# Kernel optimization log

Measured on AMD Instinct MI355X. Metric: run time of the kernel, lower is better.

The kernel has to match this reference:

```python
import jax, jax.numpy as jnp
import numpy as np

B, S = 4, 2048
N_EMBED = 1024
D_FF = 4 * N_EMBED
N_EXPERTS = 8
TOP_K = 2


def setup_inputs() -> dict:
    key = jax.random.key(0)
    ks = jax.random.split(key, 12)
    std = 0.02
    return {
        "x": jax.random.normal(ks[0], (B, S, N_EMBED), dtype=jnp.float32),
        "noise_u": jax.random.uniform(ks[1], (B, S, N_EXPERTS), dtype=jnp.float32),
        # router params
        "wg": jax.random.normal(ks[2], (N_EMBED, N_EXPERTS), dtype=jnp.float32) * std,
        "bg": jnp.zeros((N_EXPERTS,), dtype=jnp.float32),
        "wn": jax.random.normal(ks[3], (N_EMBED, N_EXPERTS), dtype=jnp.float32) * std,
        "bn": jnp.zeros((N_EXPERTS,), dtype=jnp.float32),
        # stacked expert params [E, ...]
        "w1": jax.random.normal(ks[4], (N_EXPERTS, N_EMBED, D_FF), dtype=jnp.float32) * std,
        "b1": jnp.zeros((N_EXPERTS, D_FF), dtype=jnp.float32),
        "w2": jax.random.normal(ks[5], (N_EXPERTS, D_FF, N_EMBED), dtype=jnp.float32) * std,
        "b2": jnp.zeros((N_EXPERTS, N_EMBED), dtype=jnp.float32),
    }


def reference(x, noise_u, wg, bg, wn, bn, w1, b1, w2, b2):
    # ---- NoisyTopKRouter ----
    logits = x @ wg + bg                              # [B,S,E]
    noise_logits = x @ wn + bn                        # [B,S,E]
    noisy = logits + noise_u * jax.nn.softplus(noise_logits)
    top_vals, top_idx = jax.lax.top_k(noisy, TOP_K)   # [B,S,K]
    # selected-expert mask; scatter of top-k logits == where(selected, noisy, -inf)
    sel = jax.nn.one_hot(top_idx, N_EXPERTS).sum(axis=-2) > 0   # [B,S,E] bool
    sparse_logits = jnp.where(sel, noisy, -jnp.inf)
    gates = jax.nn.softmax(sparse_logits, axis=-1)    # zero for unselected experts
    # ---- per-expert MLP, combined with gate weights (zero gate => no contribution) ----
    out = jnp.zeros_like(x)
    for e in range(N_EXPERTS):
        h = jax.nn.relu(x @ w1[e] + b1[e])            # [B,S,4d]
        y = h @ w2[e] + b2[e]                         # [B,S,d]
        out = out + gates[..., e:e + 1] * y
    return out
```

## Files before the change

### kernel.cpp

```cpp
#include <hip/hip_runtime.h>


#define T_TOK 8192
#define D_EMB 1024
#define DFF   4096
#define N_EXP 8
#define BM 128
#define BN 128
#define BK 64

typedef __attribute__((ext_vector_type(8))) short bf16x8;
typedef __attribute__((ext_vector_type(4))) float floatx4;
typedef unsigned short bf16_t;

__device__ __forceinline__ bf16_t f2bf(float f) {
  union { float f; unsigned u; } a; a.f = f;
  unsigned u = a.u;
  return (bf16_t)((u + 0x7fffu + ((u >> 16) & 1u)) >> 16);
}

__device__ __forceinline__ void gl_lds16(const bf16_t* g, bf16_t* l) {
  __builtin_amdgcn_global_load_lds(
      (const __attribute__((address_space(1))) void*)g,
      (__attribute__((address_space(3))) void*)l, 16, 0, 0);
}

__global__ __launch_bounds__(256) void cvt_x_k(const float* __restrict__ x,
                                               bf16_t* __restrict__ xb) {
  int i = (blockIdx.x * 256 + threadIdx.x) * 4;
  float4 v = *(const float4*)(x + i);
  ushort4 o;
  o.x = f2bf(v.x); o.y = f2bf(v.y); o.z = f2bf(v.z); o.w = f2bf(v.w);
  *(ushort4*)(xb + i) = o;
}

__global__ __launch_bounds__(256) void tcvt_k(const float* __restrict__ in,
                                              bf16_t* __restrict__ outp,
                                              int K, int N) {
  __shared__ float tile[32][33];
  int e  = blockIdx.z;
  int n0 = blockIdx.x * 32;
  int k0 = blockIdx.y * 32;
  int tx = threadIdx.x;
  int ty = threadIdx.y;
  const float* src = in + (size_t)e * K * N;
#pragma unroll
  for (int l = 0; l < 32; l += 8)
    tile[ty + l][tx] = src[(size_t)(k0 + ty + l) * N + (n0 + tx)];
  __syncthreads();
  bf16_t* dst = outp + (size_t)e * K * N;
#pragma unroll
  for (int l = 0; l < 32; l += 8)
    dst[(size_t)(n0 + ty + l) * K + (k0 + tx)] = f2bf(tile[tx][ty + l]);
}

__global__ __launch_bounds__(256) void router_k(
    const float* __restrict__ x, const float* __restrict__ nu,
    const float* __restrict__ wg, const float* __restrict__ bgp,
    const float* __restrict__ wn, const float* __restrict__ bnp,
    int* __restrict__ cnt, int* __restrict__ tok, float* __restrict__ gate) {
  int t = blockIdx.x;
  int tid = threadIdx.x;
  float gl[8] = {0,0,0,0,0,0,0,0};
  float nl[8] = {0,0,0,0,0,0,0,0};
  const float* xr = x + (size_t)t * D_EMB;
  for (int i = tid; i < D_EMB; i += 256) {
    float xv = xr[i];
    float4 a0 = *(const float4*)(wg + i * 8);
    float4 a1 = *(const float4*)(wg + i * 8 + 4);
    float4 c0 = *(const float4*)(wn + i * 8);
    float4 c1 = *(const float4*)(wn + i * 8 + 4);
    gl[0] += xv * a0.x; gl[1] += xv * a0.y; gl[2] += xv * a0.z; gl[3] += xv * a0.w;
    gl[4] += xv * a1.x; gl[5] += xv * a1.y; gl[6] += xv * a1.z; gl[7] += xv * a1.w;
    nl[0] += xv * c0.x; nl[1] += xv * c0.y; nl[2] += xv * c0.z; nl[3] += xv * c0.w;
    nl[4] += xv * c1.x; nl[5] += xv * c1.y; nl[6] += xv * c1.z; nl[7] += xv * c1.w;
  }
  __shared__ float red[4][16];
  int lane = tid & 63;
  int wv = tid >> 6;
#pragma unroll
  for (int o = 0; o < 16; ++o) {
    float v = (o < 8) ? gl[o] : nl[o - 8];
#pragma unroll
    for (int s = 32; s > 0; s >>= 1) v += __shfl_down(v, s, 64);
    if (lane == 0) red[wv][o] = v;
  }
  __syncthreads();
  if (tid == 0) {
    float noisy[8];
#pragma unroll
    for (int e = 0; e < 8; ++e) {
      float lg = red[0][e] + red[1][e] + red[2][e] + red[3][e] + bgp[e];
      float nz = red[0][8 + e] + red[1][8 + e] + red[2][8 + e] + red[3][8 + e] + bnp[e];
      float sp = fmaxf(nz, 0.f) + log1pf(expf(-fabsf(nz)));
      noisy[e] = lg + nu[(size_t)t * 8 + e] * sp;
    }
    int e1 = 0;
#pragma unroll
    for (int e = 1; e < 8; ++e) if (noisy[e] > noisy[e1]) e1 = e;
    int e2 = -1;
#pragma unroll
    for (int e = 0; e < 8; ++e) {
      if (e == e1) continue;
      if (e2 < 0 || noisy[e] > noisy[e2]) e2 = e;
    }
    float d = expf(noisy[e2] - noisy[e1]);
    float g1 = 1.f / (1.f + d);
    float g2 = d / (1.f + d);
    int p1 = atomicAdd(&cnt[e1], 1);
    tok[e1 * T_TOK + p1] = t; gate[e1 * T_TOK + p1] = g1;
    int p2 = atomicAdd(&cnt[e2], 1);
    tok[e2 * T_TOK + p2] = t; gate[e2 * T_TOK + p2] = g2;
  }
}

__global__ void scan_k(const int* __restrict__ cnt, int* __restrict__ offs) {
  if (threadIdx.x == 0 && blockIdx.x == 0) {
    int a = 0;
    for (int e = 0; e < N_EXP; ++e) { offs[e] = a; a += cnt[e]; }
    offs[N_EXP] = a;
  }
}

__global__ __launch_bounds__(256) void gemm1_k(
    const bf16_t* __restrict__ xb, const bf16_t* __restrict__ w1T,
    const float* __restrict__ b1p, const int* __restrict__ cnt,
    const int* __restrict__ offs, const int* __restrict__ tok,
    bf16_t* __restrict__ h) {
  const int NT = DFF / BN;
  const int MT = T_TOK / BM;
  const int NWG = N_EXP * MT * NT;
  int b0 = blockIdx.x;
  int bid = (b0 & 7) * (NWG >> 3) + (b0 >> 3);
  int e = bid / (MT * NT);
  int rem = bid % (MT * NT);
  int mt = rem / NT;
  int nt = rem % NT;
  int cnte = cnt[e];
  if (mt * BM >= cnte) return;
  int rows = min(BM, cnte - mt * BM);

  __shared__ bf16_t As[BM * BK];
  __shared__ bf16_t Bs[BN * BK];

  int tid = threadIdx.x;
  int lane = tid & 63;
  int wv = tid >> 6;
  int rq = tid >> 3;
  int c8 = tid & 7;

  const bf16_t* aptr[4];
  const bf16_t* bptr[4];
#pragma unroll
  for (int i = 0; i < 4; ++i) {
    int r = i * 32 + rq;
    int rr = (r < rows) ? r : 0;
    int t = tok[e * T_TOK + mt * BM + rr];
    int sc = ((c8 ^ (r & 7)) << 3);
    aptr[i] = xb + (size_t)t * D_EMB + sc;
    bptr[i] = w1T + ((size_t)e * DFF + nt * BN + r) * D_EMB + sc;
  }
  int ldso = wv * 512;

  int m0 = (wv & 1) * 64;
  int n0 = (wv >> 1) * 64;
  int lm = lane & 15;
  int lq = lane >> 4;
  int sw = lm & 7;

  floatx4 acc[4][4];
#pragma unroll
  for (int i = 0; i < 4; ++i)
#pragma unroll
    for (int j = 0; j < 4; ++j)
#pragma unroll
      for (int r = 0; r < 4; ++r) acc[i][j][r] = 0.f;

  for (int kk = 0; kk < D_EMB; kk += BK) {
#pragma unroll
    for (int i = 0; i < 4; ++i) gl_lds16(aptr[i] + kk, As + i * 2048 + ldso);
#pragma unroll
    for (int i = 0; i < 4; ++i) gl_lds16(bptr[i] + kk, Bs + i * 2048 + ldso);
    __syncthreads();
#pragma unroll
    for (int ks = 0; ks < BK; ks += 32) {
      int cb = (ks >> 3) + lq;
      int co = ((cb ^ sw) << 3);
      bf16x8 af[4], bfr[4];
#pragma unroll
      for (int i = 0; i < 4; ++i)
        af[i] = *(const bf16x8*)&As[(m0 + i * 16 + lm) * BK + co];
#pragma unroll
      for (int j = 0; j < 4; ++j)
        bfr[j] = *(const bf16x8*)&Bs[(n0 + j * 16 + lm) * BK + co];
#pragma unroll
      for (int i = 0; i < 4; ++i)
#pragma unroll
        for (int j = 0; j < 4; ++j)
          acc[i][j] = __builtin_amdgcn_mfma_f32_16x16x32_bf16(af[i], bfr[j], acc[i][j], 0, 0, 0);
    }
    __syncthreads();
  }

  int hbase = offs[e] + mt * BM;
#pragma unroll
  for (int i = 0; i < 4; ++i) {
    int lr0 = m0 + i * 16 + lq * 4;
#pragma unroll
    for (int r = 0; r < 4; ++r) {
      int lr = lr0 + r;
      if (lr < rows) {
        size_t hrow = (size_t)(hbase + lr) * DFF;
#pragma unroll
        for (int j = 0; j < 4; ++j) {
          int col = nt * BN + n0 + j * 16 + lm;
          float v = acc[i][j][r] + b1p[e * DFF + col];
          h[hrow + col] = f2bf(fmaxf(v, 0.f));
        }
      }
    }
  }
}

__global__ __launch_bounds__(256) void gemm2_k(
    const bf16_t* __restrict__ h, const bf16_t* __restrict__ w2T,
    const float* __restrict__ b2p, const int* __restrict__ cnt,
    const int* __restrict__ offs, const int* __restrict__ tok,
    const float* __restrict__ gate, float* __restrict__ out) {
  const int NT = D_EMB / BN;
  const int MT = T_TOK / BM;
  const int KS = 2;
  const int NWG = N_EXP * KS * MT * NT;
  int b0 = blockIdx.x;
  int bid = (b0 & 7) * (NWG >> 3) + (b0 >> 3);
  int e = bid / (KS * MT * NT);
  int rem2 = bid % (KS * MT * NT);
  int ksp = rem2 / (MT * NT);
  int rem = rem2 % (MT * NT);
  int mt = rem / NT;
  int nt = rem % NT;
  int cnte = cnt[e];
  if (mt * BM >= cnte) return;
  int rows = min(BM, cnte - mt * BM);

  __shared__ bf16_t As[BM * BK];
  __shared__ bf16_t Bs[BN * BK];
  __shared__ int stok[BM];
  __shared__ float sgate[BM];

  int tid = threadIdx.x;
  if (tid < BM) {
    int idx = e * T_TOK + mt * BM + ((tid < rows) ? tid : 0);
    stok[tid] = tok[idx];
    sgate[tid] = gate[idx];
  }

  int lane = tid & 63;
  int wv = tid >> 6;
  int rq = tid >> 3;
  int c8 = tid & 7;

  const bf16_t* aptr[4];
  const bf16_t* bptr[4];
#pragma unroll
  for (int i = 0; i < 4; ++i) {
    int r = i * 32 + rq;
    int rr = (r < rows) ? r : 0;
    int sc = ((c8 ^ (r & 7)) << 3);
    aptr[i] = h + (size_t)(offs[e] + mt * BM + rr) * DFF + sc;
    bptr[i] = w2T + ((size_t)e * D_EMB + nt * BN + r) * DFF + sc;
  }
  int ldso = wv * 512;

  int m0 = (wv & 1) * 64;
  int n0 = (wv >> 1) * 64;
  int lm = lane & 15;
  int lq = lane >> 4;
  int sw = lm & 7;

  floatx4 acc[4][4];
#pragma unroll
  for (int i = 0; i < 4; ++i)
#pragma unroll
    for (int j = 0; j < 4; ++j)
#pragma unroll
      for (int r = 0; r < 4; ++r) acc[i][j][r] = 0.f;

  int kbeg = ksp * (DFF / KS);
  int kend = kbeg + DFF / KS;
  for (int kk = kbeg; kk < kend; kk += BK) {
#pragma unroll
    for (int i = 0; i < 4; ++i) gl_lds16(aptr[i] + kk, As + i * 2048 + ldso);
#pragma unroll
    for (int i = 0; i < 4; ++i) gl_lds16(bptr[i] + kk, Bs + i * 2048 + ldso);
    __syncthreads();
#pragma unroll
    for (int ks = 0; ks < BK; ks += 32) {
      int cb = (ks >> 3) + lq;
      int co = ((cb ^ sw) << 3);
      bf16x8 af[4], bfr[4];
#pragma unroll
      for (int i = 0; i < 4; ++i)
        af[i] = *(const bf16x8*)&As[(m0 + i * 16 + lm) * BK + co];
#pragma unroll
      for (int j = 0; j < 4; ++j)
        bfr[j] = *(const bf16x8*)&Bs[(n0 + j * 16 + lm) * BK + co];
#pragma unroll
      for (int i = 0; i < 4; ++i)
#pragma unroll
        for (int j = 0; j < 4; ++j)
          acc[i][j] = __builtin_amdgcn_mfma_f32_16x16x32_bf16(af[i], bfr[j], acc[i][j], 0, 0, 0);
    }
    __syncthreads();
  }

#pragma unroll
  for (int i = 0; i < 4; ++i) {
    int lr0 = m0 + i * 16 + lq * 4;
#pragma unroll
    for (int r = 0; r < 4; ++r) {
      int lr = lr0 + r;
      if (lr < rows) {
        int t = stok[lr];
        float g = sgate[lr];
#pragma unroll
        for (int j = 0; j < 4; ++j) {
          int col = nt * BN + n0 + j * 16 + lm;
          float bb = (ksp == 0) ? b2p[e * D_EMB + col] : 0.f;
          float v = g * (acc[i][j][r] + bb);
          unsafeAtomicAdd(&out[(size_t)t * D_EMB + col], v);
        }
      }
    }
  }
}

extern "C" void kernel_launch(void* const* d_in, const int* in_sizes, int n_in,
                              void* d_out, int out_size, void* d_ws, size_t ws_size,
                              hipStream_t stream) {
  const float* x  = (const float*)d_in[0];
  const float* nu = (const float*)d_in[1];
  const float* wg = (const float*)d_in[2];
  const float* bg = (const float*)d_in[3];
  const float* wn = (const float*)d_in[4];
  const float* bn = (const float*)d_in[5];
  const float* w1 = (const float*)d_in[6];
  const float* b1 = (const float*)d_in[7];
  const float* w2 = (const float*)d_in[8];
  const float* b2 = (const float*)d_in[9];
  float* out = (float*)d_out;

  char* ws = (char*)d_ws;
  size_t o = 0;
  int* cnt  = (int*)(ws + o);
  int* offs = cnt + 8;
  o += 256;
  int*   tok  = (int*)(ws + o);   o += (size_t)N_EXP * T_TOK * 4;
  float* gate = (float*)(ws + o); o += (size_t)N_EXP * T_TOK * 4;
  bf16_t* xb  = (bf16_t*)(ws + o); o += (size_t)T_TOK * D_EMB * 2;
  bf16_t* w1T = (bf16_t*)(ws + o); o += (size_t)N_EXP * D_EMB * DFF * 2;
  bf16_t* w2T = (bf16_t*)(ws + o); o += (size_t)N_EXP * D_EMB * DFF * 2;
  bf16_t* h   = (bf16_t*)(ws + o); o += (size_t)2 * T_TOK * DFF * 2;
  (void)o; (void)ws_size; (void)in_sizes; (void)n_in;

  hipMemsetAsync(cnt, 0, 256, stream);
  hipMemsetAsync(out, 0, (size_t)out_size * sizeof(float), stream);

  cvt_x_k<<<(T_TOK * D_EMB) / 1024, 256, 0, stream>>>(x, xb);
  tcvt_k<<<dim3(DFF / 32, D_EMB / 32, N_EXP), dim3(32, 8), 0, stream>>>(w1, w1T, D_EMB, DFF);
  tcvt_k<<<dim3(D_EMB / 32, DFF / 32, N_EXP), dim3(32, 8), 0, stream>>>(w2, w2T, DFF, D_EMB);
  router_k<<<T_TOK, 256, 0, stream>>>(x, nu, wg, bg, wn, bn, cnt, tok, gate);
  scan_k<<<1, 64, 0, stream>>>(cnt, offs);
  gemm1_k<<<N_EXP * (T_TOK / BM) * (DFF / BN), 256, 0, stream>>>(xb, w1T, b1, cnt, offs, tok, h);
  gemm2_k<<<N_EXP * 2 * (T_TOK / BM) * (D_EMB / BN), 256, 0, stream>>>(h, w2T, b2, cnt, offs, tok, gate, out);
}
```

Measured before the change: 1.044 ms.

## Shrink gemm1 K tile to 32 and batch router slot atomics per block

The router now only writes each token's packed top-2 expert ids and gate pair. A new compaction kernel uses shared-memory atomics per 256-token block, then does one global atomic per expert, which cuts global atomic contention. gemm1 drops its K tile from 64 to 32 and removes the XOR swizzle, halving LDS use so more workgroups can be resident. The cost is twice as many barriers per K, possible LDS bank conflicts without the swizzle, and one extra kernel launch.

```diff
diff --git a/kernel.cpp b/kernel.cpp
--- a/kernel.cpp
+++ b/kernel.cpp
@@ -7,7 +7,6 @@
 #define N_EXP 8
 #define BM 128
 #define BN 128
-#define BK 64
 
 typedef __attribute__((ext_vector_type(8))) short bf16x8;
 typedef __attribute__((ext_vector_type(4))) float floatx4;
@@ -58,7 +57,7 @@
     const float* __restrict__ x, const float* __restrict__ nu,
     const float* __restrict__ wg, const float* __restrict__ bgp,
     const float* __restrict__ wn, const float* __restrict__ bnp,
-    int* __restrict__ cnt, int* __restrict__ tok, float* __restrict__ gate) {
+    int* __restrict__ sel, float2* __restrict__ gts) {
   int t = blockIdx.x;
   int tid = threadIdx.x;
   float gl[8] = {0,0,0,0,0,0,0,0};
@@ -107,11 +106,33 @@
     float d = expf(noisy[e2] - noisy[e1]);
     float g1 = 1.f / (1.f + d);
     float g2 = d / (1.f + d);
-    int p1 = atomicAdd(&cnt[e1], 1);
-    tok[e1 * T_TOK + p1] = t; gate[e1 * T_TOK + p1] = g1;
-    int p2 = atomicAdd(&cnt[e2], 1);
-    tok[e2 * T_TOK + p2] = t; gate[e2 * T_TOK + p2] = g2;
-  }
+    sel[t] = e1 | (e2 << 4);
+    gts[t] = make_float2(g1, g2);
+  }
+}
+
+__global__ __launch_bounds__(256) void compact_k(
+    const int* __restrict__ sel, const float2* __restrict__ gts,
+    int* __restrict__ cnt, int* __restrict__ tok, float* __restrict__ gate) {
+  __shared__ int lcnt[N_EXP];
+  __shared__ int lbase[N_EXP];
+  int tid = threadIdx.x;
+  int t = blockIdx.x * 256 + tid;
+  if (tid < N_EXP) lcnt[tid] = 0;
+  __syncthreads();
+  int pk = sel[t];
+  float2 g = gts[t];
+  int e1 = pk & 15;
+  int e2 = pk >> 4;
+  int p1 = atomicAdd(&lcnt[e1], 1);
+  int p2 = atomicAdd(&lcnt[e2], 1);
+  __syncthreads();
+  if (tid < N_EXP) lbase[tid] = atomicAdd(&cnt[tid], lcnt[tid]);
+  __syncthreads();
+  int q1 = lbase[e1] + p1;
+  int q2 = lbase[e2] + p2;
+  tok[e1 * T_TOK + q1] = t;  gate[e1 * T_TOK + q1] = g.x;
+  tok[e2 * T_TOK + q2] = t;  gate[e2 * T_TOK + q2] = g.y;
 }
 
 __global__ void scan_k(const int* __restrict__ cnt, int* __restrict__ offs) {
@@ -127,6 +148,7 @@
     const float* __restrict__ b1p, const int* __restrict__ cnt,
     const int* __restrict__ offs, const int* __restrict__ tok,
     bf16_t* __restrict__ h) {
+  const int BK1 = 32;
   const int NT = DFF / BN;
   const int MT = T_TOK / BM;
   const int NWG = N_EXP * MT * NT;
@@ -140,25 +162,24 @@
   if (mt * BM >= cnte) return;
   int rows = min(BM, cnte - mt * BM);
 
-  __shared__ bf16_t As[BM * BK];
-  __shared__ bf16_t Bs[BN * BK];
+  __shared__ bf16_t As[BM * BK1];
+  __shared__ bf16_t Bs[BN * BK1];
 
   int tid = threadIdx.x;
   int lane = tid & 63;
   int wv = tid >> 6;
-  int rq = tid >> 3;
-  int c8 = tid & 7;
-
-  const bf16_t* aptr[4];
-  const bf16_t* bptr[4];
-#pragma unroll
-  for (int i = 0; i < 4; ++i) {
-    int r = i * 32 + rq;
+  int rq = tid >> 2;
+  int c4 = tid & 3;
+
+  const bf16_t* aptr[2];
+  const bf16_t* bptr[2];
+#pragma unroll
+  for (int i = 0; i < 2; ++i) {
+    int r = i * 64 + rq;
     int rr = (r < rows) ? r : 0;
     int t = tok[e * T_TOK + mt * BM + rr];
-    int sc = ((c8 ^ (r & 7)) << 3);
-    aptr[i] = xb + (size_t)t * D_EMB + sc;
-    bptr[i] = w1T + ((size_t)e * DFF + nt * BN + r) * D_EMB + sc;
+    aptr[i] = xb + (size_t)t * D_EMB + c4 * 8;
+    bptr[i] = w1T + ((size_t)e * DFF + nt * BN + r) * D_EMB + c4 * 8;
   }
   int ldso = wv * 512;
 
@@ -166,7 +187,6 @@
   int n0 = (wv >> 1) * 64;
   int lm = lane & 15;
   int lq = lane >> 4;
-  int sw = lm & 7;
 
   floatx4 acc[4][4];
 #pragma unroll
@@ -176,29 +196,24 @@
 #pragma unroll
       for (int r = 0; r < 4; ++r) acc[i][j][r] = 0.f;
 
-  for (int kk = 0; kk < D_EMB; kk += BK) {
-#pragma unroll
-    for (int i = 0; i < 4; ++i) gl_lds16(aptr[i] + kk, As + i * 2048 + ldso);
-#pragma unroll
-    for (int i = 0; i < 4; ++i) gl_lds16(bptr[i] + kk, Bs + i * 2048 + ldso);
+  for (int kk = 0; kk < D_EMB; kk += BK1) {
+    gl_lds16(aptr[0] + kk, As + ldso);
+    gl_lds16(aptr[1] + kk, As + 2048 + ldso);
+    gl_lds16(bptr[0] + kk, Bs + ldso);
+    gl_lds16(bptr[1] + kk, Bs + 2048 + ldso);
     __syncthreads();
-#pragma unroll
-    for (int ks = 0; ks < BK; ks += 32) {
-      int cb = (ks >> 3) + lq;
-      int co = ((cb ^ sw) << 3);
-      bf16x8 af[4], bfr[4];
-#pragma unroll
-      for (int i = 0; i < 4; ++i)
-        af[i] = *(const bf16x8*)&As[(m0 + i * 16 + lm) * BK + co];
+    bf16x8 af[4], bfr[4];
+#pragma unroll
+    for (int i = 0; i < 4; ++i)
+      af[i] = *(const bf16x8*)&As[(m0 + i * 16 + lm) * BK1 + lq * 8];
+#pragma unroll
+    for (int j = 0; j < 4; ++j)
+      bfr[j] = *(const bf16x8*)&Bs[(n0 + j * 16 + lm) * BK1 + lq * 8];
+#pragma unroll
+    for (int i = 0; i < 4; ++i)
 #pragma unroll
       for (int j = 0; j < 4; ++j)
-        bfr[j] = *(const bf16x8*)&Bs[(n0 + j * 16 + lm) * BK + co];
-#pragma unroll
-      for (int i = 0; i < 4; ++i)
-#pragma unroll
-        for (int j = 0; j < 4; ++j)
-          acc[i][j] = __builtin_amdgcn_mfma_f32_16x16x32_bf16(af[i], bfr[j], acc[i][j], 0, 0, 0);
-    }
+        acc[i][j] = __builtin_amdgcn_mfma_f32_16x16x32_bf16(af[i], bfr[j], acc[i][j], 0, 0, 0);
     __syncthreads();
   }
 
@@ -227,6 +242,7 @@
     const float* __restrict__ b2p, const int* __restrict__ cnt,
     const int* __restrict__ offs, const int* __restrict__ tok,
     const float* __restrict__ gate, float* __restrict__ out) {
+  const int BK2 = 64;
   const int NT = D_EMB / BN;
   const int MT = T_TOK / BM;
   const int KS = 2;
@@ -243,8 +259,8 @@
   if (mt * BM >= cnte) return;
   int rows = min(BM, cnte - mt * BM);
 
-  __shared__ bf16_t As[BM * BK];
-  __shared__ bf16_t Bs[BN * BK];
+  __shared__ bf16_t As[BM * BK2];
+  __shared__ bf16_t Bs[BN * BK2];
   __shared__ int stok[BM];
   __shared__ float sgate[BM];
 
@@ -288,23 +304,23 @@
 
   int kbeg = ksp * (DFF / KS);
   int kend = kbeg + DFF / KS;
-  for (int kk = kbeg; kk < kend; kk += BK) {
+  for (int kk = kbeg; kk < kend; kk += BK2) {
 #pragma unroll
     for (int i = 0; i < 4; ++i) gl_lds16(aptr[i] + kk, As + i * 2048 + ldso);
 #pragma unroll
     for (int i = 0; i < 4; ++i) gl_lds16(bptr[i] + kk, Bs + i * 2048 + ldso);
     __syncthreads();
 #pragma unroll
-    for (int ks = 0; ks < BK; ks += 32) {
+    for (int ks = 0; ks < BK2; ks += 32) {
       int cb = (ks >> 3) + lq;
       int co = ((cb ^ sw) << 3);
       bf16x8 af[4], bfr[4];
 #pragma unroll
       for (int i = 0; i < 4; ++i)
-        af[i] = *(const bf16x8*)&As[(m0 + i * 16 + lm) * BK + co];
+        af[i] = *(const bf16x8*)&As[(m0 + i * 16 + lm) * BK2 + co];
 #pragma unroll
       for (int j = 0; j < 4; ++j)
-        bfr[j] = *(const bf16x8*)&Bs[(n0 + j * 16 + lm) * BK + co];
+        bfr[j] = *(const bf16x8*)&Bs[(n0 + j * 16 + lm) * BK2 + co];
 #pragma unroll
       for (int i = 0; i < 4; ++i)
 #pragma unroll
@@ -355,8 +371,10 @@
   int* cnt  = (int*)(ws + o);
   int* offs = cnt + 8;
   o += 256;
-  int*   tok  = (int*)(ws + o);   o += (size_t)N_EXP * T_TOK * 4;
-  float* gate = (float*)(ws + o); o += (size_t)N_EXP * T_TOK * 4;
+  int*    tok  = (int*)(ws + o);    o += (size_t)N_EXP * T_TOK * 4;
+  float*  gate = (float*)(ws + o);  o += (size_t)N_EXP * T_TOK * 4;
+  int*    sel  = (int*)(ws + o);    o += (size_t)T_TOK * 4;
+  float2* gts  = (float2*)(ws + o); o += (size_t)T_TOK * 8;
   bf16_t* xb  = (bf16_t*)(ws + o); o += (size_t)T_TOK * D_EMB * 2;
   bf16_t* w1T = (bf16_t*)(ws + o); o += (size_t)N_EXP * D_EMB * DFF * 2;
   bf16_t* w2T = (bf16_t*)(ws + o); o += (size_t)N_EXP * D_EMB * DFF * 2;
@@ -369,7 +387,8 @@
   cvt_x_k<<<(T_TOK * D_EMB) / 1024, 256, 0, stream>>>(x, xb);
   tcvt_k<<<dim3(DFF / 32, D_EMB / 32, N_EXP), dim3(32, 8), 0, stream>>>(w1, w1T, D_EMB, DFF);
   tcvt_k<<<dim3(D_EMB / 32, DFF / 32, N_EXP), dim3(32, 8), 0, stream>>>(w2, w2T, DFF, D_EMB);
-  router_k<<<T_TOK, 256, 0, stream>>>(x, nu, wg, bg, wn, bn, cnt, tok, gate);
+  router_k<<<T_TOK, 256, 0, stream>>>(x, nu, wg, bg, wn, bn, sel, gts);
+  compact_k<<<T_TOK / 256, 256, 0, stream>>>(sel, gts, cnt, tok, gate);
   scan_k<<<1, 64, 0, stream>>>(cnt, offs);
   gemm1_k<<<N_EXP * (T_TOK / BM) * (DFF / BN), 256, 0, stream>>>(xb, w1T, b1, cnt, offs, tok, h);
   gemm2_k<<<N_EXP * 2 * (T_TOK / BM) * (D_EMB / BN), 256, 0, stream>>>(h, w2T, b2, cnt, offs, tok, gate, out);
```

After: 865.1 us. 1.21x faster.
